# Optimization experiments

Hardware: AMD Instinct MI355X
Metric: run time of the kernel (lower is better)

## Reference

```python
import jax, jax.numpy as jnp
import numpy as np

G, N_PER, E_PER = 256, 256, 4096
F_IN, NHID, NCLS = 128, 128, 10
K1, K2, K3 = 128, 64, 32  # ceil(0.5 * prev node count)


def setup_inputs():
    key = jax.random.key(0)
    ks = jax.random.split(key, 32)
    def w(k, shape):
        fan = shape[0]
        return jax.random.normal(k, shape, jnp.float32) / np.sqrt(fan).astype(np.float32)
    return {
        "x": jax.random.normal(ks[0], (G, N_PER, F_IN), jnp.float32),
        "src": jax.random.randint(ks[1], (G, E_PER), 0, N_PER, jnp.int32),
        "dst": jax.random.randint(ks[2], (G, E_PER), 0, N_PER, jnp.int32),
        "W_root1": w(ks[3], (F_IN, NHID)), "W_rel1": w(ks[4], (F_IN, NHID)),
        "b1": jnp.zeros((NHID,), jnp.float32), "wp1": jax.random.normal(ks[5], (NHID,), jnp.float32),
        "W_root2": w(ks[6], (NHID, NHID)), "W_rel2": w(ks[7], (NHID, NHID)),
        "b2": jnp.zeros((NHID,), jnp.float32), "wp2": jax.random.normal(ks[8], (NHID,), jnp.float32),
        "W_root3": w(ks[9], (NHID, NHID)), "W_rel3": w(ks[10], (NHID, NHID)),
        "b3": jnp.zeros((NHID,), jnp.float32), "wp3": jax.random.normal(ks[11], (NHID,), jnp.float32),
        "Wl1": w(ks[12], (NHID * 2 * 3, NHID)), "bl1": jnp.zeros((NHID,), jnp.float32),
        "Wl2": w(ks[13], (NHID, NHID // 2)), "bl2": jnp.zeros((NHID // 2,), jnp.float32),
        "Wl3": w(ks[14], (NHID // 2, NCLS)), "bl3": jnp.zeros((NCLS,), jnp.float32),
    }


def graph_conv(x, src, dst, mask, W_root, W_rel, b):
    # PyG GraphConv: out_i = W_root x_i + W_rel * sum_{j->i} x_j + b
    g = x.shape[0]
    msg = jnp.take_along_axis(x, src[:, :, None], axis=1) * mask[:, :, None].astype(x.dtype)  # [G,E,F]
    agg = jnp.zeros_like(x).at[jnp.arange(g)[:, None], dst].add(msg)  # [G,N,F]
    return agg @ W_rel + x @ W_root + b


def topk_pool(x, w, src, dst, mask, k):
    # score projection, per-graph top-k node selection, gate by tanh(score)
    g, n, _ = x.shape
    score = x @ (w / jnp.linalg.norm(w))  # [G,N]
    vals, idx = jax.lax.top_k(score, k)  # [G,k]
    xk = jnp.take_along_axis(x, idx[:, :, None], axis=1) * jnp.tanh(vals)[:, :, None]
    inv = jnp.full((g, n), -1, jnp.int32).at[jnp.arange(g)[:, None], idx].set(
        jnp.broadcast_to(jnp.arange(k, dtype=jnp.int32), (g, k)))
    ns = jnp.take_along_axis(inv, src, axis=1)
    nd = jnp.take_along_axis(inv, dst, axis=1)
    nmask = mask & (ns >= 0) & (nd >= 0)
    return xk, jnp.maximum(ns, 0), jnp.maximum(nd, 0), nmask


def readout(x):
    return jnp.concatenate([x.max(axis=1), x.mean(axis=1)], axis=-1)  # [G, 2F]


def reference(x, src, dst, W_root1, W_rel1, b1, wp1, W_root2, W_rel2, b2, wp2,
              W_root3, W_rel3, b3, wp3, Wl1, bl1, Wl2, bl2, Wl3, bl3):
    mask = jnp.ones(src.shape, dtype=bool)
    h = jax.nn.relu(graph_conv(x, src, dst, mask, W_root1, W_rel1, b1))
    h, src, dst, mask = topk_pool(h, wp1, src, dst, mask, K1)
    r1 = readout(h)
    h = jax.nn.relu(graph_conv(h, src, dst, mask, W_root2, W_rel2, b2))
    h, src, dst, mask = topk_pool(h, wp2, src, dst, mask, K2)
    r2 = readout(h)
    h = jax.nn.relu(graph_conv(h, src, dst, mask, W_root3, W_rel3, b3))
    h, src, dst, mask = topk_pool(h, wp3, src, dst, mask, K3)
    r3 = readout(h)
    z = jnp.concatenate([r1, r2, r3], axis=-1)  # [G, 6*NHID]
    z = jax.nn.relu(z @ Wl1 + bl1)
    # dropout is identity in eval mode
    z = jax.nn.relu(z @ Wl2 + bl2)
    return jax.nn.log_softmax(z @ Wl3 + bl3, axis=-1)
```

## Files before the change

### kernel.cpp

```cpp
#include <hip/hip_runtime.h>
#include <cstdint>
#include <cstddef>

#define G 256
#define EPER 4096
#define F 128
#define TILE_U32 16384

typedef __attribute__((ext_vector_type(8))) short short8;
typedef __attribute__((ext_vector_type(4))) float f32x4;

__device__ inline unsigned short f2bf(float f) {
    unsigned u = __float_as_uint(f);
    u += 0x7FFFu + ((u >> 16) & 1u);
    return (unsigned short)(u >> 16);
}
__device__ inline float bf2f(unsigned short b) { return __uint_as_float(((unsigned)b) << 16); }

__device__ inline void unpack2(uint4 qa, uint4 qb, short8& h1, short8& h2) {
    h1[0] = (short)qa.x; h2[0] = (short)(qa.x >> 16);
    h1[1] = (short)qa.y; h2[1] = (short)(qa.y >> 16);
    h1[2] = (short)qa.z; h2[2] = (short)(qa.z >> 16);
    h1[3] = (short)qa.w; h2[3] = (short)(qa.w >> 16);
    h1[4] = (short)qb.x; h2[4] = (short)(qb.x >> 16);
    h1[5] = (short)qb.y; h2[5] = (short)(qb.y >> 16);
    h1[6] = (short)qb.z; h2[6] = (short)(qb.z >> 16);
    h1[7] = (short)qb.w; h2[7] = (short)(qb.w >> 16);
}

__global__ __launch_bounds__(256) void k_wsplit(const float* __restrict__ Wr1, const float* __restrict__ Wl1,
                                                const float* __restrict__ Wr2, const float* __restrict__ Wl2,
                                                const float* __restrict__ Wr3, const float* __restrict__ Wl3,
                                                unsigned short* __restrict__ Wf) {
    int gid = blockIdx.x * 256 + threadIdx.x;
    int s = gid >> 15;
    int idx = gid & 32767;
    int j = idx & 7, col = (idx >> 3) & 127, ko = idx >> 10;
    int k = ko * 8 + j;
    const float* Wr = (s == 0) ? Wr1 : (s == 1) ? Wr2 : Wr3;
    const float* Wl = (s == 0) ? Wl1 : (s == 1) ? Wl2 : Wl3;
    float f = (k < 128) ? Wr[(size_t)k * 128 + col] : Wl[(size_t)(k - 128) * 128 + col];
    unsigned short h1 = f2bf(f), h2 = f2bf(f - bf2f(h1));
    Wf[(size_t)s * 65536 + idx] = h1;
    Wf[(size_t)s * 65536 + 32768 + idx] = h2;
}

__global__ __launch_bounds__(1024) void k_stage1(const float* __restrict__ X,
                                                 const int* __restrict__ src,
                                                 const int* __restrict__ dst,
                                                 const float* __restrict__ wp,
                                                 const float* __restrict__ bias,
                                                 const unsigned short* __restrict__ Wf,
                                                 int* __restrict__ cmap,
                                                 float* __restrict__ R,
                                                 unsigned* __restrict__ XF,
                                                 unsigned* __restrict__ AGGF1,
                                                 unsigned* __restrict__ AGGF2) {
    __shared__ __align__(16) char smem[107520];
    __shared__ float sc[256];
    __shared__ unsigned long long keys[256];
    __shared__ int sel[128];
    __shared__ int inv[256];
    __shared__ float wn[128];
    __shared__ float gates[128];
    __shared__ float pmx[8 * 128];
    __shared__ float psm[8 * 128];
    __shared__ int ncm[256];
    __shared__ float snorm_s;

    const int g = blockIdx.x, t = threadIdx.x;
    const int lane = t & 63, wv = t >> 6;
    const int l15 = lane & 15, lko = lane >> 4;

    if (t < 64) {
        float v = wp[t] * wp[t] + wp[t + 64] * wp[t + 64];
        #pragma unroll
        for (int o = 32; o; o >>= 1) v += __shfl_xor(v, o);
        if (t == 0) snorm_s = sqrtf(v);
    }

    {
        unsigned* adjc = (unsigned*)smem;
        short* adjT = (short*)(smem + 65536);
        short* xsA = (short*)(smem + 81920);
        constexpr int NS = 256, NS4 = 64;
        {
            uint4* z = (uint4*)adjc;
            #pragma unroll
            for (int i = t; i < NS * NS4 / 4; i += 1024) z[i] = uint4{0, 0, 0, 0};
        }
        __syncthreads();
        if (t < 128) wn[t] = wp[t] / snorm_s;

        const int* sg = src + (size_t)g * EPER;
        const int* dg = dst + (size_t)g * EPER;
        #pragma unroll
        for (int j = 0; j < 4; ++j) {
            int e = j * 1024 + t;
            int s = sg[e], d = dg[e];
            int pos = (s + 4 * d) & (NS - 1);
            __hip_atomic_fetch_add(&adjc[d * NS4 + (pos >> 2)], 1u << ((pos & 3) * 8),
                                   __ATOMIC_RELAXED, __HIP_MEMORY_SCOPE_WORKGROUP);
        }

        f32x4 acc[8];
        #pragma unroll
        for (int c = 0; c < 8; ++c) acc[c] = f32x4{0.f, 0.f, 0.f, 0.f};
        const int mA = t >> 2, kgA = (t & 3) * 8;
        const int nX = t & 127, oX = (t >> 7) & 3;

        for (int k0 = 0; k0 < NS; k0 += 32) {
            __syncthreads();
            {
                unsigned short cs[8];
                #pragma unroll
                for (int q = 0; q < 2; ++q) {
                    unsigned w = adjc[mA * NS4 + ((((k0 + kgA) >> 2) + mA + q) & (NS4 - 1))];
                    cs[q * 4 + 0] = f2bf((float)(w & 255u));
                    cs[q * 4 + 1] = f2bf((float)((w >> 8) & 255u));
                    cs[q * 4 + 2] = f2bf((float)((w >> 16) & 255u));
                    cs[q * 4 + 3] = f2bf((float)(w >> 24));
                }
                short8 w8;
                #pragma unroll
                for (int j = 0; j < 8; ++j) w8[j] = (short)cs[j];
                *(short8*)&adjT[(t & 3) * NS * 8 + mA * 8] = w8;
            }
            if (t < 512) {
                short8 h1, h2;
                #pragma unroll
                for (int j = 0; j < 8; ++j) {
                    float f = X[(size_t)g * 32768 + (size_t)(k0 + oX * 8 + j) * F + nX];
                    unsigned short a1 = f2bf(f);
                    unsigned short a2 = f2bf(f - bf2f(a1));
                    h1[j] = (short)a1; h2[j] = (short)a2;
                }
                *(short8*)&xsA[oX * 1024 + nX * 8] = h1;
                *(short8*)&xsA[4096 + oX * 1024 + nX * 8] = h2;
            }
            __syncthreads();
            short8 afr = *(const short8*)&adjT[lko * NS * 8 + (wv * 16 + l15) * 8];
            #pragma unroll
            for (int s = 0; s < 2; ++s) {
                #pragma unroll
                for (int ct = 0; ct < 8; ++ct) {
                    short8 bfr = *(const short8*)&xsA[s * 4096 + lko * 1024 + (ct * 16 + l15) * 8];
                    acc[ct] = __builtin_amdgcn_mfma_f32_16x16x32_bf16(afr, bfr, acc[ct], 0, 0, 0);
                }
            }
        }

        #pragma unroll
        for (int ct = 0; ct < 8; ++ct) {
            int feat = ct * 16 + l15;
            size_t fb = (size_t)(feat >> 3) * 1024 + (feat & 7);
            int r0 = wv * 16 + lko * 4;
            #pragma unroll
            for (int r = 0; r < 4; ++r) {
                int m = g * NS + r0 + r;
                float v = acc[ct][r];
                unsigned short hi = f2bf(v);
                unsigned short lo = f2bf(v - bf2f(hi));
                AGGF1[(size_t)(m >> 7) * TILE_U32 + fb + (size_t)(m & 127) * 8] =
                    (unsigned)hi | ((unsigned)lo << 16);
            }
        }
    }
    __syncthreads();

    f32x4 acc2[8];
    {
        uint4* Whi = (uint4*)smem;
        uint4* Afs = (uint4*)(smem + 65536);
        const unsigned short* Wlo = Wf + 32768;
        {
            const uint4* Wf4 = (const uint4*)Wf;
            #pragma unroll
            for (int i = 0; i < 4; ++i) Whi[t + i * 1024] = Wf4[t + i * 1024];
        }
        #pragma unroll
        for (int c = 0; c < 8; ++c) acc2[c] = f32x4{0.f, 0.f, 0.f, 0.f};

        const int rs = t >> 2, ck = t & 3;
        const int rowp = t & 255, kop = t >> 8;

        for (int kt = 0; kt < 8; ++kt) {
            __syncthreads();
            if (kt < 4) {
                const float* srow = X + (size_t)g * 32768 + (size_t)rs * 128 + kt * 32 + ck * 8;
                float4 fa = *(const float4*)srow;
                float4 fb = *(const float4*)(srow + 4);
                float vv[8] = {fa.x, fa.y, fa.z, fa.w, fb.x, fb.y, fb.z, fb.w};
                short8 h1, h2;
                #pragma unroll
                for (int j = 0; j < 8; ++j) {
                    unsigned short a1 = f2bf(vv[j]);
                    unsigned short a2 = f2bf(vv[j] - bf2f(a1));
                    h1[j] = (short)a1; h2[j] = (short)a2;
                }
                int rw = rs ^ (ck << 2);
                *reinterpret_cast<short8*>(&Afs[(0 * 4 + ck) * 256 + rw]) = h1;
                *reinterpret_cast<short8*>(&Afs[(1 * 4 + ck) * 256 + rw]) = h2;
            } else {
                int ko = (kt & 3) * 4 + kop;
                int tile = 2 * g + (rowp >> 7);
                size_t idx = (size_t)tile * TILE_U32 + (size_t)ko * 1024 + (size_t)(rowp & 127) * 8;
                uint4 qa = *(const uint4*)(AGGF1 + idx);
                uint4 qb = *(const uint4*)(AGGF1 + idx + 4);
                short8 h1, h2;
                unpack2(qa, qb, h1, h2);
                int rw = rowp ^ (kop << 2);
                *reinterpret_cast<short8*>(&Afs[(0 * 4 + kop) * 256 + rw]) = h1;
                *reinterpret_cast<short8*>(&Afs[(1 * 4 + kop) * 256 + rw]) = h2;
            }
            __syncthreads();

            int row = (wv * 16 + l15) ^ (lko << 2);
            short8 a1f = *reinterpret_cast<const short8*>(&Afs[(0 * 4 + lko) * 256 + row]);
            short8 a2f = *reinterpret_cast<const short8*>(&Afs[(1 * 4 + lko) * 256 + row]);
            const int kog = kt * 4 + lko;
            #pragma unroll
            for (int ct = 0; ct < 8; ++ct) {
                int col = ct * 16 + l15;
                short8 w1 = *reinterpret_cast<const short8*>(&Whi[kog * 128 + col]);
                short8 w2 = *reinterpret_cast<const short8*>(Wlo + ((size_t)kog * 128 + col) * 8);
                acc2[ct] = __builtin_amdgcn_mfma_f32_16x16x32_bf16(a1f, w1, acc2[ct], 0, 0, 0);
                acc2[ct] = __builtin_amdgcn_mfma_f32_16x16x32_bf16(a2f, w1, acc2[ct], 0, 0, 0);
                acc2[ct] = __builtin_amdgcn_mfma_f32_16x16x32_bf16(a1f, w2, acc2[ct], 0, 0, 0);
            }
        }
    }
    __syncthreads();

    #pragma unroll
    for (int ct = 0; ct < 8; ++ct) {
        float bv = bias[ct * 16 + l15];
        #pragma unroll
        for (int r = 0; r < 4; ++r) acc2[ct][r] = fmaxf(acc2[ct][r] + bv, 0.f);
    }

    {
        unsigned* adjc2 = (unsigned*)(smem + 66560);
        for (int i = t; i < 4096; i += 1024) adjc2[i] = 0;
        float wnv[8];
        #pragma unroll
        for (int ct = 0; ct < 8; ++ct) wnv[ct] = wn[ct * 16 + l15];
        #pragma unroll
        for (int r = 0; r < 4; ++r) {
            float p = 0.f;
            #pragma unroll
            for (int ct = 0; ct < 8; ++ct) p += acc2[ct][r] * wnv[ct];
            p += __shfl_xor(p, 1); p += __shfl_xor(p, 2);
            p += __shfl_xor(p, 4); p += __shfl_xor(p, 8);
            if (l15 == 0) sc[wv * 16 + lko * 4 + r] = p;
        }
    }
    __syncthreads();

    if (t < 256) {
        unsigned u = __float_as_uint(sc[t]);
        u = (u & 0x80000000u) ? ~u : (u | 0x80000000u);
        keys[t] = ((unsigned long long)u << 32) | (unsigned)(~t);
    }
    __syncthreads();
    for (int kk = 2; kk <= 256; kk <<= 1) {
        for (int j = kk >> 1; j > 0; j >>= 1) {
            if (t < 256) {
                int ixj = t ^ j;
                if (ixj > t) {
                    unsigned long long a = keys[t], b = keys[ixj];
                    bool up = (t & kk) == 0;
                    if (up ? (a < b) : (a > b)) { keys[t] = b; keys[ixj] = a; }
                }
            }
            __syncthreads();
        }
    }
    if (t < 128) sel[t] = (int)(~(unsigned)keys[t]);
    if (t < 256) inv[t] = -1;
    __syncthreads();
    if (t < 128) {
        inv[sel[t]] = t;
        gates[t] = tanhf(sc[sel[t]]);
    }
    __syncthreads();
    if (t < 256) {
        int nc = inv[t];
        ncm[t] = nc;
        cmap[g * 256 + t] = nc;
    }
    __syncthreads();

    {
        unsigned* hp = (unsigned*)smem;
        #pragma unroll
        for (int r = 0; r < 4; ++r) {
            int rowg = wv * 16 + lko * 4 + r;
            int j = inv[rowg];
            if (j >= 0) {
                float gt = gates[j];
                #pragma unroll
                for (int ct = 0; ct < 8; ++ct) {
                    float v = acc2[ct][r] * gt;
                    unsigned short hi = f2bf(v);
                    unsigned short lo = f2bf(v - bf2f(hi));
                    hp[j * 130 + ct * 16 + l15] = (unsigned)hi | ((unsigned)lo << 16);
                }
            }
        }
    }
    __syncthreads();

    {
        unsigned* hp = (unsigned*)smem;
        unsigned* adjc2 = (unsigned*)(smem + 66560);
        short* adjT2 = (short*)(smem + 82944);
        short* xs2 = (short*)(smem + 91136);
        constexpr int K = 128, NS4 = 32;

        {
            const int* sg = src + (size_t)g * EPER;
            const int* dg = dst + (size_t)g * EPER;
            #pragma unroll
            for (int j = 0; j < 4; ++j) {
                int e = j * 1024 + t;
                int s = ncm[sg[e]], d = ncm[dg[e]];
                if (s >= 0 && d >= 0) {
                    int pos = (s + 4 * d) & (K - 1);
                    __hip_atomic_fetch_add(&adjc2[d * NS4 + (pos >> 2)], 1u << ((pos & 3) * 8),
                                           __ATOMIC_RELAXED, __HIP_MEMORY_SCOPE_WORKGROUP);
                }
            }
        }
        {
            const int f = t & 127, seg = t >> 7;
            float mx = -INFINITY, sm = 0.f;
            for (int j = seg; j < K; j += 8) {
                unsigned u = hp[j * 130 + f];
                float v = bf2f((unsigned short)(u & 0xffffu)) + bf2f((unsigned short)(u >> 16));
                mx = fmaxf(mx, v);
                sm += v;
            }
            pmx[seg * 128 + f] = mx;
            psm[seg * 128 + f] = sm;
        }
        for (int i = t; i < K * F; i += 1024) {
            int j = i >> 7, f = i & 127;
            int m = g * K + j;
            XF[(size_t)(m >> 7) * TILE_U32 + (size_t)(f >> 3) * 1024 + (size_t)(m & 127) * 8 + (f & 7)] =
                hp[j * 130 + f];
        }
        __syncthreads();
        if (t < 128) {
            float m = -INFINITY, s = 0.f;
            #pragma unroll
            for (int q = 0; q < 8; ++q) {
                m = fmaxf(m, pmx[q * 128 + t]);
                s += psm[q * 128 + t];
            }
            R[(size_t)g * 768 + t] = m;
            R[(size_t)g * 768 + 128 + t] = s * (1.0f / K);
        }

        const int rt = wv >> 1, cq = wv & 1;
        f32x4 acc3[4];
        #pragma unroll
        for (int c = 0; c < 4; ++c) acc3[c] = f32x4{0.f, 0.f, 0.f, 0.f};

        for (int k0 = 0; k0 < K; k0 += 32) {
            __syncthreads();
            if (t < K * 4) {
                const int m = t >> 2, kg = (t & 3) * 8;
                unsigned short cs[8];
                #pragma unroll
                for (int q = 0; q < 2; ++q) {
                    unsigned w = adjc2[m * NS4 + ((((k0 + kg) >> 2) + m + q) & (NS4 - 1))];
                    cs[q * 4 + 0] = f2bf((float)(w & 255u));
                    cs[q * 4 + 1] = f2bf((float)((w >> 8) & 255u));
                    cs[q * 4 + 2] = f2bf((float)((w >> 16) & 255u));
                    cs[q * 4 + 3] = f2bf((float)(w >> 24));
                }
                short8 w8;
                #pragma unroll
                for (int j = 0; j < 8; ++j) w8[j] = (short)cs[j];
                *(short8*)&adjT2[(t & 3) * K * 8 + m * 8] = w8;
            }
            if (t >= 512) {
                const int feat = t & 127, o = (t >> 7) & 3;
                short8 h1, h2;
                #pragma unroll
                for (int j = 0; j < 8; ++j) {
                    unsigned u = hp[(k0 + o * 8 + j) * 130 + feat];
                    h1[j] = (short)(u & 0xffffu);
                    h2[j] = (short)(u >> 16);
                }
                *(short8*)&xs2[o * 1024 + feat * 8] = h1;
                *(short8*)&xs2[4096 + o * 1024 + feat * 8] = h2;
            }
            __syncthreads();

            short8 afr = *(const short8*)&adjT2[lko * K * 8 + (rt * 16 + l15) * 8];
            #pragma unroll
            for (int s = 0; s < 2; ++s) {
                #pragma unroll
                for (int ct = 0; ct < 4; ++ct) {
                    int feat = cq * 64 + ct * 16 + l15;
                    short8 bfr = *(const short8*)&xs2[s * 4096 + lko * 1024 + feat * 8];
                    acc3[ct] = __builtin_amdgcn_mfma_f32_16x16x32_bf16(afr, bfr, acc3[ct], 0, 0, 0);
                }
            }
        }

        #pragma unroll
        for (int ct = 0; ct < 4; ++ct) {
            int feat = cq * 64 + ct * 16 + l15;
            size_t fb = (size_t)(feat >> 3) * 1024 + (feat & 7);
            int r0 = rt * 16 + lko * 4;
            #pragma unroll
            for (int r = 0; r < 4; ++r) {
                int m = g * K + r0 + r;
                float v = acc3[ct][r];
                unsigned short hi = f2bf(v);
                unsigned short lo = f2bf(v - bf2f(hi));
                AGGF2[(size_t)(m >> 7) * TILE_U32 + fb + (size_t)(m & 127) * 8] =
                    (unsigned)hi | ((unsigned)lo << 16);
            }
        }
    }
}

__global__ __launch_bounds__(1024) void k_stage2(const int* __restrict__ src,
                                                 const int* __restrict__ dst,
                                                 const float* __restrict__ wp,
                                                 const float* __restrict__ bias,
                                                 const unsigned short* __restrict__ Wf,
                                                 const int* __restrict__ cmap,
                                                 float* __restrict__ R,
                                                 const unsigned* __restrict__ XF,
                                                 const unsigned* __restrict__ AGGF,
                                                 unsigned* __restrict__ XF2,
                                                 unsigned* __restrict__ AGGF3) {
    __shared__ __align__(16) char smem[81920];
    __shared__ float sc[128];
    __shared__ unsigned long long keys[128];
    __shared__ int sel[64];
    __shared__ int inv[128];
    __shared__ float wn[128];
    __shared__ float gates[64];
    __shared__ float scp[2][128];
    __shared__ float pmx[8 * 128];
    __shared__ float psm[8 * 128];
    __shared__ int ncm[256];
    __shared__ float snorm_s;

    const int g = blockIdx.x, t = threadIdx.x;
    const int lane = t & 63, wv = t >> 6;
    const int l15 = lane & 15, lko = lane >> 4;
    const int rt = wv >> 1, cq = wv & 1;

    if (t < 64) {
        float v = wp[t] * wp[t] + wp[t + 64] * wp[t + 64];
        #pragma unroll
        for (int o = 32; o; o >>= 1) v += __shfl_xor(v, o);
        if (t == 0) snorm_s = sqrtf(v);
    }
    __syncthreads();
    if (t < 128) wn[t] = wp[t] / snorm_s;

    f32x4 acc2[4];
    {
        uint4* Whi = (uint4*)smem;
        uint4* Afs = (uint4*)(smem + 65536);
        const unsigned short* Wlo = Wf + 32768;
        {
            const uint4* Wf4 = (const uint4*)Wf;
            #pragma unroll
            for (int i = 0; i < 4; ++i) Whi[t + i * 1024] = Wf4[t + i * 1024];
        }
        #pragma unroll
        for (int c = 0; c < 4; ++c) acc2[c] = f32x4{0.f, 0.f, 0.f, 0.f};

        const int rowp = t & 127, kop = (t >> 7) & 3;

        for (int kt = 0; kt < 8; ++kt) {
            __syncthreads();
            if (t < 512) {
                const unsigned* P = (kt < 4) ? XF : AGGF;
                int ko = (kt & 3) * 4 + kop;
                size_t idx = (size_t)g * TILE_U32 + (size_t)ko * 1024 + (size_t)rowp * 8;
                uint4 qa = *(const uint4*)(P + idx);
                uint4 qb = *(const uint4*)(P + idx + 4);
                short8 h1, h2;
                unpack2(qa, qb, h1, h2);
                int rw = rowp ^ (kop << 2);
                *reinterpret_cast<short8*>(&Afs[(0 * 4 + kop) * 128 + rw]) = h1;
                *reinterpret_cast<short8*>(&Afs[(1 * 4 + kop) * 128 + rw]) = h2;
            }
            __syncthreads();

            int row = (rt * 16 + l15) ^ (lko << 2);
            short8 a1f = *reinterpret_cast<const short8*>(&Afs[(0 * 4 + lko) * 128 + row]);
            short8 a2f = *reinterpret_cast<const short8*>(&Afs[(1 * 4 + lko) * 128 + row]);
            const int kog = kt * 4 + lko;
            #pragma unroll
            for (int ct = 0; ct < 4; ++ct) {
                int col = cq * 64 + ct * 16 + l15;
                short8 w1 = *reinterpret_cast<const short8*>(&Whi[kog * 128 + col]);
                short8 w2 = *reinterpret_cast<const short8*>(Wlo + ((size_t)kog * 128 + col) * 8);
                acc2[ct] = __builtin_amdgcn_mfma_f32_16x16x32_bf16(a1f, w1, acc2[ct], 0, 0, 0);
                acc2[ct] = __builtin_amdgcn_mfma_f32_16x16x32_bf16(a2f, w1, acc2[ct], 0, 0, 0);
                acc2[ct] = __builtin_amdgcn_mfma_f32_16x16x32_bf16(a1f, w2, acc2[ct], 0, 0, 0);
            }
        }
    }
    __syncthreads();

    #pragma unroll
    for (int ct = 0; ct < 4; ++ct) {
        float bv = bias[cq * 64 + ct * 16 + l15];
        #pragma unroll
        for (int r = 0; r < 4; ++r) acc2[ct][r] = fmaxf(acc2[ct][r] + bv, 0.f);
    }

    {
        float wnv[4];
        #pragma unroll
        for (int ct = 0; ct < 4; ++ct) wnv[ct] = wn[cq * 64 + ct * 16 + l15];
        #pragma unroll
        for (int r = 0; r < 4; ++r) {
            float p = 0.f;
            #pragma unroll
            for (int ct = 0; ct < 4; ++ct) p += acc2[ct][r] * wnv[ct];
            p += __shfl_xor(p, 1); p += __shfl_xor(p, 2);
            p += __shfl_xor(p, 4); p += __shfl_xor(p, 8);
            if (l15 == 0) scp[cq][rt * 16 + lko * 4 + r] = p;
        }
    }
    {
        unsigned* adjc3 = (unsigned*)(smem + 33280);
        if (t < 1024) adjc3[t] = 0;
    }
    __syncthreads();
    if (t < 128) sc[t] = scp[0][t] + scp[1][t];
    __syncthreads();

    if (t < 128) {
        unsigned u = __float_as_uint(sc[t]);
        u = (u & 0x80000000u) ? ~u : (u | 0x80000000u);
        keys[t] = ((unsigned long long)u << 32) | (unsigned)(~t);
    }
    __syncthreads();
    for (int kk = 2; kk <= 128; kk <<= 1) {
        for (int j = kk >> 1; j > 0; j >>= 1) {
            if (t < 128) {
                int ixj = t ^ j;
                if (ixj > t) {
                    unsigned long long a = keys[t], b = keys[ixj];
                    bool up = (t & kk) == 0;
                    if (up ? (a < b) : (a > b)) { keys[t] = b; keys[ixj] = a; }
                }
            }
            __syncthreads();
        }
    }
    if (t < 64) sel[t] = (int)(~(unsigned)keys[t]);
    if (t < 128) inv[t] = -1;
    __syncthreads();
    if (t < 64) {
        inv[sel[t]] = t;
        gates[t] = tanhf(sc[sel[t]]);
    }
    __syncthreads();
    if (t < 256) {
        int c = cmap[g * 256 + t];
        ncm[t] = (c >= 0) ? inv[c] : -1;
    }
    __syncthreads();

    {
        unsigned* hp = (unsigned*)smem;
        #pragma unroll
        for (int r = 0; r < 4; ++r) {
            int rowg = rt * 16 + lko * 4 + r;
            int j = inv[rowg];
            if (j >= 0) {
                float gt = gates[j];
                #pragma unroll
                for (int ct = 0; ct < 4; ++ct) {
                    float v = acc2[ct][r] * gt;
                    unsigned short hi = f2bf(v);
                    unsigned short lo = f2bf(v - bf2f(hi));
                    hp[j * 130 + cq * 64 + ct * 16 + l15] = (unsigned)hi | ((unsigned)lo << 16);
                }
            }
        }
    }
    __syncthreads();

    {
        unsigned* hp = (unsigned*)smem;
        unsigned* adjc3 = (unsigned*)(smem + 33280);
        short* adjT3 = (short*)(smem + 37376);
        short* xs3 = (short*)(smem + 41472);
        constexpr int K = 64, NS4 = 16;

        {
            const int* sg = src + (size_t)g * EPER;
            const int* dg = dst + (size_t)g * EPER;
            #pragma unroll
            for (int j = 0; j < 4; ++j) {
                int e = j * 1024 + t;
                int s = ncm[sg[e]], d = ncm[dg[e]];
                if (s >= 0 && d >= 0) {
                    int pos = (s + 4 * d) & (K - 1);
                    __hip_atomic_fetch_add(&adjc3[d * NS4 + (pos >> 2)], 1u << ((pos & 3) * 8),
                                           __ATOMIC_RELAXED, __HIP_MEMORY_SCOPE_WORKGROUP);
                }
            }
        }
        {
            const int f = t & 127, seg = t >> 7;
            float mx = -INFINITY, sm = 0.f;
            for (int j = seg; j < K; j += 8) {
                unsigned u = hp[j * 130 + f];
                float v = bf2f((unsigned short)(u & 0xffffu)) + bf2f((unsigned short)(u >> 16));
                mx = fmaxf(mx, v);
                sm += v;
            }
            pmx[seg * 128 + f] = mx;
            psm[seg * 128 + f] = sm;
        }
        for (int i = t; i < K * F; i += 1024) {
            int j = i >> 7, f = i & 127;
            int m = g * K + j;
            XF2[(size_t)(m >> 7) * TILE_U32 + (size_t)(f >> 3) * 1024 + (size_t)(m & 127) * 8 + (f & 7)] =
                hp[j * 130 + f];
        }
        __syncthreads();
        if (t < 128) {
            float m = -INFINITY, s = 0.f;
            #pragma unroll
            for (int q = 0; q < 8; ++q) {
                m = fmaxf(m, pmx[q * 128 + t]);
                s += psm[q * 128 + t];
            }
            R[(size_t)g * 768 + 256 + t] = m;
            R[(size_t)g * 768 + 384 + t] = s * (1.0f / K);
        }

        const int rt3 = wv >> 2, cq3 = wv & 3;
        f32x4 acc3[2];
        acc3[0] = f32x4{0.f, 0.f, 0.f, 0.f};
        acc3[1] = f32x4{0.f, 0.f, 0.f, 0.f};

        for (int k0 = 0; k0 < K; k0 += 32) {
            __syncthreads();
            if (t < K * 4) {
                const int m = t >> 2, kg = (t & 3) * 8;
                unsigned short cs[8];
                #pragma unroll
                for (int q = 0; q < 2; ++q) {
                    unsigned w = adjc3[m * NS4 + ((((k0 + kg) >> 2) + m + q) & (NS4 - 1))];
                    cs[q * 4 + 0] = f2bf((float)(w & 255u));
                    cs[q * 4 + 1] = f2bf((float)((w >> 8) & 255u));
                    cs[q * 4 + 2] = f2bf((float)((w >> 16) & 255u));
                    cs[q * 4 + 3] = f2bf((float)(w >> 24));
                }
                short8 w8;
                #pragma unroll
                for (int j = 0; j < 8; ++j) w8[j] = (short)cs[j];
                *(short8*)&adjT3[(t & 3) * K * 8 + m * 8] = w8;
            }
            if (t >= 512) {
                const int feat = t & 127, o = (t >> 7) & 3;
                short8 h1, h2;
                #pragma unroll
                for (int j = 0; j < 8; ++j) {
                    unsigned u = hp[(k0 + o * 8 + j) * 130 + feat];
                    h1[j] = (short)(u & 0xffffu);
                    h2[j] = (short)(u >> 16);
                }
                *(short8*)&xs3[o * 1024 + feat * 8] = h1;
                *(short8*)&xs3[4096 + o * 1024 + feat * 8] = h2;
            }
            __syncthreads();

            short8 afr = *(const short8*)&adjT3[lko * K * 8 + (rt3 * 16 + l15) * 8];
            #pragma unroll
            for (int s = 0; s < 2; ++s) {
                #pragma unroll
                for (int ct = 0; ct < 2; ++ct) {
                    int feat = cq3 * 32 + ct * 16 + l15;
                    short8 bfr = *(const short8*)&xs3[s * 4096 + lko * 1024 + feat * 8];
                    acc3[ct] = __builtin_amdgcn_mfma_f32_16x16x32_bf16(afr, bfr, acc3[ct], 0, 0, 0);
                }
            }
        }

        #pragma unroll
        for (int ct = 0; ct < 2; ++ct) {
            int feat = cq3 * 32 + ct * 16 + l15;
            size_t fb = (size_t)(feat >> 3) * 1024 + (feat & 7);
            int r0 = rt3 * 16 + lko * 4;
            #pragma unroll
            for (int r = 0; r < 4; ++r) {
                int m = g * K + r0 + r;
                float v = acc3[ct][r];
                unsigned short hi = f2bf(v);
                unsigned short lo = f2bf(v - bf2f(hi));
                AGGF3[(size_t)(m >> 7) * TILE_U32 + fb + (size_t)(m & 127) * 8] =
                    (unsigned)hi | ((unsigned)lo << 16);
            }
        }
    }
}

__global__ __launch_bounds__(1024) void k_stage3(const float* __restrict__ wp,
                                                 const float* __restrict__ bias,
                                                 const unsigned short* __restrict__ Wf,
                                                 const float* __restrict__ R,
                                                 const unsigned* __restrict__ XF2,
                                                 const unsigned* __restrict__ AGGF3,
                                                 const float* __restrict__ W1, const float* __restrict__ b1,
                                                 const float* __restrict__ W2, const float* __restrict__ b2,
                                                 const float* __restrict__ W3, const float* __restrict__ b3,
                                                 float* __restrict__ out) {
    __shared__ __align__(16) char smem[73728];
    __shared__ float sc[64];
    __shared__ unsigned long long keys[64];
    __shared__ int sel[32];
    __shared__ int inv[64];
    __shared__ float wn[128];
    __shared__ float gates[32];
    __shared__ float scp[4][64];
    __shared__ float pmx[8 * 128];
    __shared__ float psm[8 * 128];
    __shared__ float z[768];
    __shared__ float part[8][128];
    __shared__ float z2[128];
    __shared__ float z3[64];
    __shared__ float lg[10];
    __shared__ float lse;
    __shared__ float snorm_s;

    const int g = blockIdx.x, t = threadIdx.x;
    const int lane = t & 63, wv = t >> 6;
    const int l15 = lane & 15, lko = lane >> 4;
    const int rt = wv >> 2, cq = wv & 3;

    if (t < 64) {
        float v = wp[t] * wp[t] + wp[t + 64] * wp[t + 64];
        #pragma unroll
        for (int o = 32; o; o >>= 1) v += __shfl_xor(v, o);
        if (t == 0) snorm_s = sqrtf(v);
    }
    __syncthreads();
    if (t < 128) wn[t] = wp[t] / snorm_s;
    if (t < 512) z[t] = R[(size_t)g * 768 + t];

    f32x4 acc2[2];
    {
        uint4* Whi = (uint4*)smem;
        uint4* Afs = (uint4*)(smem + 65536);
        const unsigned short* Wlo = Wf + 32768;
        {
            const uint4* Wf4 = (const uint4*)Wf;
            #pragma unroll
            for (int i = 0; i < 4; ++i) Whi[t + i * 1024] = Wf4[t + i * 1024];
        }
        acc2[0] = f32x4{0.f, 0.f, 0.f, 0.f};
        acc2[1] = f32x4{0.f, 0.f, 0.f, 0.f};

        const int rowp = t & 63, kop = (t >> 6) & 3;

        for (int kt = 0; kt < 8; ++kt) {
            __syncthreads();
            if (t < 256) {
                const unsigned* P = (kt < 4) ? XF2 : AGGF3;
                int ko = (kt & 3) * 4 + kop;
                size_t idx = (size_t)(g >> 1) * TILE_U32 + (size_t)ko * 1024
                           + (size_t)((g & 1) * 64 + rowp) * 8;
                uint4 qa = *(const uint4*)(P + idx);
                uint4 qb = *(const uint4*)(P + idx + 4);
                short8 h1, h2;
                unpack2(qa, qb, h1, h2);
                int rw = rowp ^ (kop << 2);
                *reinterpret_cast<short8*>(&Afs[(0 * 4 + kop) * 64 + rw]) = h1;
                *reinterpret_cast<short8*>(&Afs[(1 * 4 + kop) * 64 + rw]) = h2;
            }
            __syncthreads();

            int row = (rt * 16 + l15) ^ (lko << 2);
            short8 a1f = *reinterpret_cast<const short8*>(&Afs[(0 * 4 + lko) * 64 + row]);
            short8 a2f = *reinterpret_cast<const short8*>(&Afs[(1 * 4 + lko) * 64 + row]);
            const int kog = kt * 4 + lko;
            #pragma unroll
            for (int ct = 0; ct < 2; ++ct) {
                int col = cq * 32 + ct * 16 + l15;
                short8 w1 = *reinterpret_cast<const short8*>(&Whi[kog * 128 + col]);
                short8 w2 = *reinterpret_cast<const short8*>(Wlo + ((size_t)kog * 128 + col) * 8);
                acc2[ct] = __builtin_amdgcn_mfma_f32_16x16x32_bf16(a1f, w1, acc2[ct], 0, 0, 0);
                acc2[ct] = __builtin_amdgcn_mfma_f32_16x16x32_bf16(a2f, w1, acc2[ct], 0, 0, 0);
                acc2[ct] = __builtin_amdgcn_mfma_f32_16x16x32_bf16(a1f, w2, acc2[ct], 0, 0, 0);
            }
        }
    }
    __syncthreads();

    #pragma unroll
    for (int ct = 0; ct < 2; ++ct) {
        float bv = bias[cq * 32 + ct * 16 + l15];
        #pragma unroll
        for (int r = 0; r < 4; ++r) acc2[ct][r] = fmaxf(acc2[ct][r] + bv, 0.f);
    }

    {
        float wnv[2];
        wnv[0] = wn[cq * 32 + l15];
        wnv[1] = wn[cq * 32 + 16 + l15];
        #pragma unroll
        for (int r = 0; r < 4; ++r) {
            float p = acc2[0][r] * wnv[0] + acc2[1][r] * wnv[1];
            p += __shfl_xor(p, 1); p += __shfl_xor(p, 2);
            p += __shfl_xor(p, 4); p += __shfl_xor(p, 8);
            if (l15 == 0) scp[cq][rt * 16 + lko * 4 + r] = p;
        }
    }
    __syncthreads();
    if (t < 64) sc[t] = scp[0][t] + scp[1][t] + scp[2][t] + scp[3][t];
    __syncthreads();

    if (t < 64) {
        unsigned u = __float_as_uint(sc[t]);
        u = (u & 0x80000000u) ? ~u : (u | 0x80000000u);
        keys[t] = ((unsigned long long)u << 32) | (unsigned)(~t);
    }
    __syncthreads();
    for (int kk = 2; kk <= 64; kk <<= 1) {
        for (int j = kk >> 1; j > 0; j >>= 1) {
            if (t < 64) {
                int ixj = t ^ j;
                if (ixj > t) {
                    unsigned long long a = keys[t], b = keys[ixj];
                    bool up = (t & kk) == 0;
                    if (up ? (a < b) : (a > b)) { keys[t] = b; keys[ixj] = a; }
                }
            }
            __syncthreads();
        }
    }
    if (t < 32) sel[t] = (int)(~(unsigned)keys[t]);
    if (t < 64) inv[t] = -1;
    __syncthreads();
    if (t < 32) {
        inv[sel[t]] = t;
        gates[t] = tanhf(sc[sel[t]]);
    }
    __syncthreads();

    {
        unsigned* hp = (unsigned*)smem;
        #pragma unroll
        for (int r = 0; r < 4; ++r) {
            int rowg = rt * 16 + lko * 4 + r;
            int j = inv[rowg];
            if (j >= 0) {
                float gt = gates[j];
                #pragma unroll
                for (int ct = 0; ct < 2; ++ct) {
                    float v = acc2[ct][r] * gt;
                    unsigned short hi = f2bf(v);
                    unsigned short lo = f2bf(v - bf2f(hi));
                    hp[j * 130 + cq * 32 + ct * 16 + l15] = (unsigned)hi | ((unsigned)lo << 16);
                }
            }
        }
    }
    __syncthreads();

    {
        unsigned* hp = (unsigned*)smem;
        const int f = t & 127, seg = t >> 7;
        float mx = -INFINITY, sm = 0.f;
        for (int j = seg; j < 32; j += 8) {
            unsigned u = hp[j * 130 + f];
            float v = bf2f((unsigned short)(u & 0xffffu)) + bf2f((unsigned short)(u >> 16));
            mx = fmaxf(mx, v);
            sm += v;
        }
        pmx[seg * 128 + f] = mx;
        psm[seg * 128 + f] = sm;
    }
    __syncthreads();
    if (t < 128) {
        float m = -INFINITY, s = 0.f;
        #pragma unroll
        for (int q = 0; q < 8; ++q) {
            m = fmaxf(m, pmx[q * 128 + t]);
            s += psm[q * 128 + t];
        }
        z[512 + t] = m;
        z[640 + t] = s * (1.0f / 32);
    }
    __syncthreads();

    {
        const int f = t & 127, seg = t >> 7;
        float acc = 0.f;
        const float* w = W1 + (size_t)(seg * 96) * 128 + f;
        const float* zz = z + seg * 96;
        #pragma unroll 8
        for (int k = 0; k < 96; ++k) acc = fmaf(zz[k], w[(size_t)k * 128], acc);
        part[seg][f] = acc;
    }
    __syncthreads();
    if (t < 128) {
        float a = b1[t];
        #pragma unroll
        for (int q = 0; q < 8; ++q) a += part[q][t];
        z2[t] = fmaxf(a, 0.f);
    }
    __syncthreads();
    if (t < 512) {
        const int f = t & 63, seg = t >> 6;
        float acc = 0.f;
        const float* w = W2 + (size_t)(seg * 16) * 64 + f;
        const float* zz = z2 + seg * 16;
        #pragma unroll
        for (int k = 0; k < 16; ++k) acc = fmaf(zz[k], w[(size_t)k * 64], acc);
        part[seg][f] = acc;
    }
    __syncthreads();
    if (t < 64) {
        float a = b2[t];
        #pragma unroll
        for (int q = 0; q < 8; ++q) a += part[q][t];
        z3[t] = fmaxf(a, 0.f);
    }
    __syncthreads();
    if (t < 10) {
        float a3 = b3[t];
        #pragma unroll 8
        for (int k = 0; k < 64; ++k) a3 = fmaf(z3[k], W3[(size_t)k * 10 + t], a3);
        lg[t] = a3;
    }
    __syncthreads();
    if (t == 0) {
        float m = lg[0];
        for (int c = 1; c < 10; ++c) m = fmaxf(m, lg[c]);
        float s = 0.f;
        for (int c = 0; c < 10; ++c) s += expf(lg[c] - m);
        lse = m + logf(s);
    }
    __syncthreads();
    if (t < 10) out[(size_t)g * 10 + t] = lg[t] - lse;
}

extern "C" void kernel_launch(void* const* d_in, const int* in_sizes, int n_in,
                              void* d_out, int out_size, void* d_ws, size_t ws_size,
                              hipStream_t stream) {
    (void)in_sizes; (void)n_in; (void)out_size; (void)ws_size;
    const float* x    = (const float*)d_in[0];
    const int*   src  = (const int*)d_in[1];
    const int*   dst  = (const int*)d_in[2];
    const float* Wr1  = (const float*)d_in[3];
    const float* Wrel1= (const float*)d_in[4];
    const float* b1   = (const float*)d_in[5];
    const float* wp1  = (const float*)d_in[6];
    const float* Wr2  = (const float*)d_in[7];
    const float* Wrel2= (const float*)d_in[8];
    const float* b2   = (const float*)d_in[9];
    const float* wp2  = (const float*)d_in[10];
    const float* Wr3  = (const float*)d_in[11];
    const float* Wrel3= (const float*)d_in[12];
    const float* b3   = (const float*)d_in[13];
    const float* wp3  = (const float*)d_in[14];
    const float* L1w  = (const float*)d_in[15];
    const float* L1b  = (const float*)d_in[16];
    const float* L2w  = (const float*)d_in[17];
    const float* L2b  = (const float*)d_in[18];
    const float* L3w  = (const float*)d_in[19];
    const float* L3b  = (const float*)d_in[20];

    int*      cmap  = (int*)d_ws;
    float*    R     = (float*)(cmap + (size_t)G * 256);
    unsigned* AGGF1 = (unsigned*)(R + (size_t)G * 768);
    unsigned* AGGF2 = AGGF1 + (size_t)G * 2 * TILE_U32;
    unsigned* XF    = AGGF2 + (size_t)G * TILE_U32;
    unsigned* XF2   = XF + (size_t)G * TILE_U32;
    unsigned* AGGF3 = XF2 + (size_t)(G / 2) * TILE_U32;
    unsigned short* Wf = (unsigned short*)(AGGF3 + (size_t)(G / 2) * TILE_U32);
    float* out = (float*)d_out;

    k_wsplit<<<384, 256, 0, stream>>>(Wr1, Wrel1, Wr2, Wrel2, Wr3, Wrel3, Wf);

    k_stage1<<<G, 1024, 0, stream>>>(x, src, dst, wp1, b1, Wf, cmap, R, XF, AGGF1, AGGF2);
    k_stage2<<<G, 1024, 0, stream>>>(src, dst, wp2, b2, Wf + 65536, cmap, R, XF, AGGF2, XF2, AGGF3);
    k_stage3<<<G, 1024, 0, stream>>>(wp3, b3, Wf + 131072, R, XF2, AGGF3,
                                     L1w, L1b, L2w, L2b, L3w, L3b, out);
}
```

Before: 118.4 us.

## Keep stage-1 aggregation in registers and double-buffer LDS tiles instead of global round-trip

The first GraphConv aggregation result is no longer written to a global AGGF1 buffer and read back. Accumulators stay in registers and are fed into the second GEMM's LDS staging buffer directly. Both the adjacency×X GEMM and the root/rel GEMM now double-buffer their LDS tiles with register prefetch of the next X chunk, which halves the barriers per iteration. The adjacency fragments are built straight from the packed count matrix using a cheap exact byte-to-bf16 conversion, so no transposed copy is needed. Shared memory grows to 144 KB, which may limit occupancy or exceed the LDS budget.

New measurement: 112.8 us. 4.7% less time.

```diff
diff --git a/kernel.cpp b/kernel.cpp
--- a/kernel.cpp
+++ b/kernel.cpp
@@ -8,6 +8,7 @@
 #define TILE_U32 16384
 
 typedef __attribute__((ext_vector_type(8))) short short8;
+typedef __attribute__((ext_vector_type(4))) short s16x4;
 typedef __attribute__((ext_vector_type(4))) float f32x4;
 
 __device__ inline unsigned short f2bf(float f) {
@@ -26,6 +27,10 @@
     h1[5] = (short)qb.y; h2[5] = (short)(qb.y >> 16);
     h1[6] = (short)qb.z; h2[6] = (short)(qb.z >> 16);
     h1[7] = (short)qb.w; h2[7] = (short)(qb.w >> 16);
+}
+
+__device__ inline short u8bf(unsigned byte) {
+    return (short)(__float_as_uint((float)byte) >> 16);
 }
 
 __global__ __launch_bounds__(256) void k_wsplit(const float* __restrict__ Wr1, const float* __restrict__ Wl1,
@@ -54,9 +59,8 @@
                                                  int* __restrict__ cmap,
                                                  float* __restrict__ R,
                                                  unsigned* __restrict__ XF,
-                                                 unsigned* __restrict__ AGGF1,
                                                  unsigned* __restrict__ AGGF2) {
-    __shared__ __align__(16) char smem[107520];
+    __shared__ __align__(16) char smem[147456];
     __shared__ float sc[256];
     __shared__ unsigned long long keys[256];
     __shared__ int sel[128];
@@ -79,15 +83,15 @@
         if (t == 0) snorm_s = sqrtf(v);
     }
 
+    f32x4 acc[8];
+
     {
         unsigned* adjc = (unsigned*)smem;
-        short* adjT = (short*)(smem + 65536);
-        short* xsA = (short*)(smem + 81920);
-        constexpr int NS = 256, NS4 = 64;
+        short* xsA = (short*)(smem + 65536);
         {
             uint4* z = (uint4*)adjc;
             #pragma unroll
-            for (int i = t; i < NS * NS4 / 4; i += 1024) z[i] = uint4{0, 0, 0, 0};
+            for (int i = t; i < 4096; i += 1024) z[i] = uint4{0, 0, 0, 0};
         }
         __syncthreads();
         if (t < 128) wn[t] = wp[t] / snorm_s;
@@ -98,80 +102,88 @@
         for (int j = 0; j < 4; ++j) {
             int e = j * 1024 + t;
             int s = sg[e], d = dg[e];
-            int pos = (s + 4 * d) & (NS - 1);
-            __hip_atomic_fetch_add(&adjc[d * NS4 + (pos >> 2)], 1u << ((pos & 3) * 8),
+            int pos = (s + 8 * d) & 255;
+            __hip_atomic_fetch_add(&adjc[d * 64 + (pos >> 2)], 1u << ((pos & 3) * 8),
                                    __ATOMIC_RELAXED, __HIP_MEMORY_SCOPE_WORKGROUP);
         }
 
-        f32x4 acc[8];
         #pragma unroll
         for (int c = 0; c < 8; ++c) acc[c] = f32x4{0.f, 0.f, 0.f, 0.f};
-        const int mA = t >> 2, kgA = (t & 3) * 8;
-        const int nX = t & 127, oX = (t >> 7) & 3;
-
-        for (int k0 = 0; k0 < NS; k0 += 32) {
-            __syncthreads();
+
+        const float* Xg = X + (size_t)g * 32768;
+        const int feat = t & 127, ko2 = (t >> 7) & 3, jh = t >> 9;
+        const int stoff = ko2 * 1024 + feat * 8 + jh * 4;
+
+        {
+            float v[4];
+            #pragma unroll
+            for (int i = 0; i < 4; ++i)
+                v[i] = Xg[(size_t)(ko2 * 8 + jh * 4 + i) * F + feat];
+            s16x4 h1, h2;
+            #pragma unroll
+            for (int i = 0; i < 4; ++i) {
+                unsigned short a1 = f2bf(v[i]);
+                unsigned short a2 = f2bf(v[i] - bf2f(a1));
+                h1[i] = (short)a1; h2[i] = (short)a2;
+            }
+            *(s16x4*)&xsA[stoff] = h1;
+            *(s16x4*)&xsA[4096 + stoff] = h2;
+        }
+        __syncthreads();
+
+        for (int kt = 0; kt < 8; ++kt) {
+            const int b = kt & 1;
+            float v[4];
+            if (kt < 7) {
+                int k0n = (kt + 1) * 32;
+                #pragma unroll
+                for (int i = 0; i < 4; ++i)
+                    v[i] = Xg[(size_t)(k0n + ko2 * 8 + jh * 4 + i) * F + feat];
+            }
             {
-                unsigned short cs[8];
-                #pragma unroll
-                for (int q = 0; q < 2; ++q) {
-                    unsigned w = adjc[mA * NS4 + ((((k0 + kgA) >> 2) + mA + q) & (NS4 - 1))];
-                    cs[q * 4 + 0] = f2bf((float)(w & 255u));
-                    cs[q * 4 + 1] = f2bf((float)((w >> 8) & 255u));
-                    cs[q * 4 + 2] = f2bf((float)((w >> 16) & 255u));
-                    cs[q * 4 + 3] = f2bf((float)(w >> 24));
-                }
-                short8 w8;
-                #pragma unroll
-                for (int j = 0; j < 8; ++j) w8[j] = (short)cs[j];
-                *(short8*)&adjT[(t & 3) * NS * 8 + mA * 8] = w8;
-            }
-            if (t < 512) {
-                short8 h1, h2;
-                #pragma unroll
-                for (int j = 0; j < 8; ++j) {
-                    float f = X[(size_t)g * 32768 + (size_t)(k0 + oX * 8 + j) * F + nX];
-                    unsigned short a1 = f2bf(f);
-                    unsigned short a2 = f2bf(f - bf2f(a1));
-                    h1[j] = (short)a1; h2[j] = (short)a2;
-                }
-                *(short8*)&xsA[oX * 1024 + nX * 8] = h1;
-                *(short8*)&xsA[4096 + oX * 1024 + nX * 8] = h2;
-            }
-            __syncthreads();
-            short8 afr = *(const short8*)&adjT[lko * NS * 8 + (wv * 16 + l15) * 8];
-            #pragma unroll
-            for (int s = 0; s < 2; ++s) {
-                #pragma unroll
-                for (int ct = 0; ct < 8; ++ct) {
-                    short8 bfr = *(const short8*)&xsA[s * 4096 + lko * 1024 + (ct * 16 + l15) * 8];
-                    acc[ct] = __builtin_amdgcn_mfma_f32_16x16x32_bf16(afr, bfr, acc[ct], 0, 0, 0);
-                }
-            }
-        }
-
-        #pragma unroll
-        for (int ct = 0; ct < 8; ++ct) {
-            int feat = ct * 16 + l15;
-            size_t fb = (size_t)(feat >> 3) * 1024 + (feat & 7);
-            int r0 = wv * 16 + lko * 4;
-            #pragma unroll
-            for (int r = 0; r < 4; ++r) {
-                int m = g * NS + r0 + r;
-                float v = acc[ct][r];
-                unsigned short hi = f2bf(v);
-                unsigned short lo = f2bf(v - bf2f(hi));
-                AGGF1[(size_t)(m >> 7) * TILE_U32 + fb + (size_t)(m & 127) * 8] =
-                    (unsigned)hi | ((unsigned)lo << 16);
-            }
-        }
-    }
-    __syncthreads();
+                int m = wv * 16 + l15;
+                int pos = ((kt * 32 + lko * 8) + 8 * m) & 255;
+                unsigned w0 = adjc[m * 64 + (pos >> 2)];
+                unsigned w1 = adjc[m * 64 + (pos >> 2) + 1];
+                short8 afr;
+                afr[0] = u8bf(w0 & 255u);
+                afr[1] = u8bf((w0 >> 8) & 255u);
+                afr[2] = u8bf((w0 >> 16) & 255u);
+                afr[3] = u8bf(w0 >> 24);
+                afr[4] = u8bf(w1 & 255u);
+                afr[5] = u8bf((w1 >> 8) & 255u);
+                afr[6] = u8bf((w1 >> 16) & 255u);
+                afr[7] = u8bf(w1 >> 24);
+                const short* xb = xsA + b * 8192;
+                #pragma unroll
+                for (int s = 0; s < 2; ++s) {
+                    #pragma unroll
+                    for (int ct = 0; ct < 8; ++ct) {
+                        short8 bfr = *(const short8*)&xb[s * 4096 + lko * 1024 + (ct * 16 + l15) * 8];
+                        acc[ct] = __builtin_amdgcn_mfma_f32_16x16x32_bf16(afr, bfr, acc[ct], 0, 0, 0);
+                    }
+                }
+            }
+            if (kt < 7) {
+                s16x4 h1, h2;
+                #pragma unroll
+                for (int i = 0; i < 4; ++i) {
+                    unsigned short a1 = f2bf(v[i]);
+                    unsigned short a2 = f2bf(v[i] - bf2f(a1));
+                    h1[i] = (short)a1; h2[i] = (short)a2;
+                }
+                short* xo = xsA + (b ^ 1) * 8192;
+                *(s16x4*)&xo[stoff] = h1;
+                *(s16x4*)&xo[4096 + stoff] = h2;
+            }
+            __syncthreads();
+        }
+    }
 
     f32x4 acc2[8];
     {
         uint4* Whi = (uint4*)smem;
-        uint4* Afs = (uint4*)(smem + 65536);
+        unsigned* AGP = (unsigned*)(smem + 65536);
         const unsigned short* Wlo = Wf + 32768;
         {
             const uint4* Wf4 = (const uint4*)Wf;
@@ -182,55 +194,84 @@
         for (int c = 0; c < 8; ++c) acc2[c] = f32x4{0.f, 0.f, 0.f, 0.f};
 
         const int rs = t >> 2, ck = t & 3;
-        const int rowp = t & 255, kop = t >> 8;
+        const float* Xg = X + (size_t)g * 32768;
+
+        {
+            const float* srow = Xg + (size_t)rs * F + ck * 8;
+            float4 fa = *(const float4*)srow;
+            float4 fb = *(const float4*)(srow + 4);
+            float vv[8] = {fa.x, fa.y, fa.z, fa.w, fb.x, fb.y, fb.z, fb.w};
+            unsigned q[8];
+            #pragma unroll
+            for (int j = 0; j < 8; ++j) {
+                unsigned short hi = f2bf(vv[j]);
+                unsigned short lo = f2bf(vv[j] - bf2f(hi));
+                q[j] = (unsigned)hi | ((unsigned)lo << 16);
+            }
+            unsigned* d0 = AGP + rs * 36 + ck * 8;
+            *(uint4*)d0 = uint4{q[0], q[1], q[2], q[3]};
+            *(uint4*)(d0 + 4) = uint4{q[4], q[5], q[6], q[7]};
+        }
+        __syncthreads();
 
         for (int kt = 0; kt < 8; ++kt) {
-            __syncthreads();
-            if (kt < 4) {
-                const float* srow = X + (size_t)g * 32768 + (size_t)rs * 128 + kt * 32 + ck * 8;
-                float4 fa = *(const float4*)srow;
-                float4 fb = *(const float4*)(srow + 4);
-                float vv[8] = {fa.x, fa.y, fa.z, fa.w, fb.x, fb.y, fb.z, fb.w};
-                short8 h1, h2;
-                #pragma unroll
-                for (int j = 0; j < 8; ++j) {
-                    unsigned short a1 = f2bf(vv[j]);
-                    unsigned short a2 = f2bf(vv[j] - bf2f(a1));
-                    h1[j] = (short)a1; h2[j] = (short)a2;
-                }
-                int rw = rs ^ (ck << 2);
-                *reinterpret_cast<short8*>(&Afs[(0 * 4 + ck) * 256 + rw]) = h1;
-                *reinterpret_cast<short8*>(&Afs[(1 * 4 + ck) * 256 + rw]) = h2;
-            } else {
-                int ko = (kt & 3) * 4 + kop;
-                int tile = 2 * g + (rowp >> 7);
-                size_t idx = (size_t)tile * TILE_U32 + (size_t)ko * 1024 + (size_t)(rowp & 127) * 8;
-                uint4 qa = *(const uint4*)(AGGF1 + idx);
-                uint4 qb = *(const uint4*)(AGGF1 + idx + 4);
-                short8 h1, h2;
-                unpack2(qa, qb, h1, h2);
-                int rw = rowp ^ (kop << 2);
-                *reinterpret_cast<short8*>(&Afs[(0 * 4 + kop) * 256 + rw]) = h1;
-                *reinterpret_cast<short8*>(&Afs[(1 * 4 + kop) * 256 + rw]) = h2;
-            }
-            __syncthreads();
-
-            int row = (wv * 16 + l15) ^ (lko << 2);
-            short8 a1f = *reinterpret_cast<const short8*>(&Afs[(0 * 4 + lko) * 256 + row]);
-            short8 a2f = *reinterpret_cast<const short8*>(&Afs[(1 * 4 + lko) * 256 + row]);
-            const int kog = kt * 4 + lko;
-            #pragma unroll
-            for (int ct = 0; ct < 8; ++ct) {
-                int col = ct * 16 + l15;
-                short8 w1 = *reinterpret_cast<const short8*>(&Whi[kog * 128 + col]);
-                short8 w2 = *reinterpret_cast<const short8*>(Wlo + ((size_t)kog * 128 + col) * 8);
-                acc2[ct] = __builtin_amdgcn_mfma_f32_16x16x32_bf16(a1f, w1, acc2[ct], 0, 0, 0);
-                acc2[ct] = __builtin_amdgcn_mfma_f32_16x16x32_bf16(a2f, w1, acc2[ct], 0, 0, 0);
-                acc2[ct] = __builtin_amdgcn_mfma_f32_16x16x32_bf16(a1f, w2, acc2[ct], 0, 0, 0);
-            }
-        }
-    }
-    __syncthreads();
+            const int b = kt & 1;
+            float4 fa, fb;
+            if (kt < 3) {
+                const float* srow = Xg + (size_t)rs * F + (kt + 1) * 32 + ck * 8;
+                fa = *(const float4*)srow;
+                fb = *(const float4*)(srow + 4);
+            }
+            {
+                int row = wv * 16 + l15;
+                const unsigned* ag = AGP + b * 9216 + row * 36 + lko * 8;
+                uint4 qa = *(const uint4*)ag;
+                uint4 qb = *(const uint4*)(ag + 4);
+                short8 a1f, a2f;
+                unpack2(qa, qb, a1f, a2f);
+                const int kog = kt * 4 + lko;
+                #pragma unroll
+                for (int ct = 0; ct < 8; ++ct) {
+                    int col = ct * 16 + l15;
+                    short8 w1 = *(const short8*)&Whi[kog * 128 + col];
+                    short8 w2 = *(const short8*)(Wlo + ((size_t)kog * 128 + col) * 8);
+                    acc2[ct] = __builtin_amdgcn_mfma_f32_16x16x32_bf16(a1f, w1, acc2[ct], 0, 0, 0);
+                    acc2[ct] = __builtin_amdgcn_mfma_f32_16x16x32_bf16(a2f, w1, acc2[ct], 0, 0, 0);
+                    acc2[ct] = __builtin_amdgcn_mfma_f32_16x16x32_bf16(a1f, w2, acc2[ct], 0, 0, 0);
+                }
+            }
+            if (kt < 7) {
+                unsigned* dstb = AGP + (b ^ 1) * 9216;
+                if (kt < 3) {
+                    float vv[8] = {fa.x, fa.y, fa.z, fa.w, fb.x, fb.y, fb.z, fb.w};
+                    unsigned q[8];
+                    #pragma unroll
+                    for (int j = 0; j < 8; ++j) {
+                        unsigned short hi = f2bf(vv[j]);
+                        unsigned short lo = f2bf(vv[j] - bf2f(hi));
+                        q[j] = (unsigned)hi | ((unsigned)lo << 16);
+                    }
+                    unsigned* d0 = dstb + rs * 36 + ck * 8;
+                    *(uint4*)d0 = uint4{q[0], q[1], q[2], q[3]};
+                    *(uint4*)(d0 + 4) = uint4{q[4], q[5], q[6], q[7]};
+                } else {
+                    int ct0 = (kt - 3) * 2;
+                    #pragma unroll
+                    for (int r = 0; r < 4; ++r) {
+                        int rowo = wv * 16 + lko * 4 + r;
+                        #pragma unroll
+                        for (int h = 0; h < 2; ++h) {
+                            float vv = acc[ct0 + h][r];
+                            unsigned short hi = f2bf(vv);
+                            unsigned short lo = f2bf(vv - bf2f(hi));
+                            dstb[rowo * 36 + h * 16 + l15] = (unsigned)hi | ((unsigned)lo << 16);
+                        }
+                    }
+                }
+            }
+            __syncthreads();
+        }
+    }
 
     #pragma unroll
     for (int ct = 0; ct < 8; ++ct) {
@@ -984,8 +1025,7 @@
 
     int*      cmap  = (int*)d_ws;
     float*    R     = (float*)(cmap + (size_t)G * 256);
-    unsigned* AGGF1 = (unsigned*)(R + (size_t)G * 768);
-    unsigned* AGGF2 = AGGF1 + (size_t)G * 2 * TILE_U32;
+    unsigned* AGGF2 = (unsigned*)(R + (size_t)G * 768);
     unsigned* XF    = AGGF2 + (size_t)G * TILE_U32;
     unsigned* XF2   = XF + (size_t)G * TILE_U32;
     unsigned* AGGF3 = XF2 + (size_t)(G / 2) * TILE_U32;
@@ -994,7 +1034,7 @@
 
     k_wsplit<<<384, 256, 0, stream>>>(Wr1, Wrel1, Wr2, Wrel2, Wr3, Wrel3, Wf);
 
-    k_stage1<<<G, 1024, 0, stream>>>(x, src, dst, wp1, b1, Wf, cmap, R, XF, AGGF1, AGGF2);
+    k_stage1<<<G, 1024, 0, stream>>>(x, src, dst, wp1, b1, Wf, cmap, R, XF, AGGF2);
     k_stage2<<<G, 1024, 0, stream>>>(src, dst, wp2, b2, Wf + 65536, cmap, R, XF, AGGF2, XF2, AGGF3);
     k_stage3<<<G, 1024, 0, stream>>>(wp3, b3, Wf + 131072, R, XF2, AGGF3,
                                      L1w, L1b, L2w, L2b, L3w, L3b, out);
```
